# Optimization experiments

Measured on AMD Instinct MI355X. Metric: run time of the kernel, lower is better.

Reference implementation:

```python
import jax, jax.numpy as jnp
import numpy as np

MOE_TOP_K = 2
MOE_GATE_NORM_STD = 1.0  # moe_gate_norm_std


def setup_inputs() -> dict:
    key = jax.random.key(0)
    k1, k2, k3, k4 = jax.random.split(key, 4)
    T, D, E = 16384, 2048, 8
    return {
        "x": jax.random.normal(k1, (T, D), dtype=jnp.float32),
        "wg_weight": jax.random.normal(k2, (E, D), dtype=jnp.float32) * 0.02,
        "gate_map_weight": jax.random.normal(k3, (E, E), dtype=jnp.float32) * 0.1,
        "gate_residual": jax.random.normal(k4, (T, E), dtype=jnp.float32),
    }


def reference(x, wg_weight, gate_map_weight, gate_residual):
    # Router GEMM in fp32 (module force-casts wg and input to float32)
    logits = jnp.einsum("td,ed->te", x.astype(jnp.float32), wg_weight)  # [T, E]
    # gate_residual path: gate_map Linear(E, E, bias=False)
    logits = logits + jnp.einsum("te,fe->tf", gate_residual, gate_map_weight)

    num_experts = wg_weight.shape[0]
    # gating(): moe_use_mixtral_gating=False, moe_use_logits_norm=True
    # torch.std is unbiased (ddof=1)
    logits_std = jnp.std(logits, axis=1, keepdims=True, ddof=1)
    probs = jax.nn.softmax(logits / (logits_std / MOE_GATE_NORM_STD), axis=1)
    gates, indices = jax.lax.top_k(probs, MOE_TOP_K)  # [T, K]
    # zero out routing to the last expert, then renormalize
    gates = jnp.where(indices == num_experts - 1, jnp.zeros_like(gates), gates)
    gates = gates / jnp.sum(gates, axis=1, keepdims=True)
    # Dense equivalent of the per-expert nonzero-gather dict: (indices, gates)
    # fully determines expert_info[e] = (tokens where indices==e, matching gates).
    return gates, indices, logits
```

## Files before the change

### kernel.cpp

```cpp
#include <hip/hip_runtime.h>
#include <hip/hip_bf16.h>
#include <stdint.h>


#define TOKENS_PER_WAVE 4
#define WAVES_PER_BLOCK 4
#define TOKENS_PER_BLOCK (TOKENS_PER_WAVE * WAVES_PER_BLOCK)
#define DCONST 2048
#define HALF_D 1024

__device__ __forceinline__ unsigned long long shfl_xor_u64(unsigned long long v, int m) {
    int lo = __shfl_xor((int)(uint32_t)v, m, 64);
    int hi = __shfl_xor((int)(uint32_t)(v >> 32), m, 64);
    return ((unsigned long long)(uint32_t)hi << 32) | (unsigned long long)(uint32_t)lo;
}

__global__ __launch_bounds__(256, 4)
void router_kernel(const float* __restrict__ x,
                   const float* __restrict__ wg,
                   const float* __restrict__ gm,
                   const float* __restrict__ gr,
                   float* __restrict__ out,
                   int T)
{
    const int wave = threadIdx.x >> 6;
    const int lane = threadIdx.x & 63;
    const int t0   = blockIdx.x * TOKENS_PER_BLOCK + wave * TOKENS_PER_WAVE;

    __shared__ float swg[8 * HALF_D];

    float acc[32];
    #pragma unroll
    for (int v = 0; v < 32; ++v) acc[v] = 0.f;

    const float* xw = x + (size_t)t0 * DCONST + (lane << 2);
    const float* wl = swg + (lane << 2);

    float4 xa[TOKENS_PER_WAVE], xb[TOKENS_PER_WAVE];

    #define LOADX(buf, g)                                                     \
        { _Pragma("unroll")                                                   \
          for (int tt = 0; tt < TOKENS_PER_WAVE; ++tt)                        \
              buf[tt] = *(const float4*)(xw + tt * DCONST + (g) * 256); }

    #define COMPUTE(j, buf)                                                   \
        { _Pragma("unroll")                                                   \
          for (int e = 0; e < 8; ++e) {                                       \
              const float4 wf = *(const float4*)(wl + e * HALF_D + (j) * 256);\
              _Pragma("unroll")                                               \
              for (int tt = 0; tt < TOKENS_PER_WAVE; ++tt) {                  \
                  acc[tt * 8 + e] += buf[tt].x * wf.x;                        \
                  acc[tt * 8 + e] += buf[tt].y * wf.y;                        \
                  acc[tt * 8 + e] += buf[tt].z * wf.z;                        \
                  acc[tt * 8 + e] += buf[tt].w * wf.w;                        \
              }                                                               \
          } }

    #pragma unroll 1
    for (int p = 0; p < 2; ++p) {
        if (p) __syncthreads();
        {
            const float4* src = (const float4*)wg;
            float4*       dst = (float4*)swg;
            #pragma unroll
            for (int i = 0; i < 8; ++i) {
                const int idx = threadIdx.x + i * 256;
                const int e   = idx >> 8;
                const int c4  = idx & 255;
                dst[idx] = src[e * 512 + p * 256 + c4];
            }
        }
        __syncthreads();

        const int g0 = p * 4;
        LOADX(xa, g0);
        LOADX(xb, g0 + 1);
        COMPUTE(0, xa);
        LOADX(xa, g0 + 2);
        COMPUTE(1, xb);
        LOADX(xb, g0 + 3);
        COMPUTE(2, xa);
        COMPUTE(3, xb);
    }

    #pragma unroll
    for (int m = 1; m < 32; m <<= 1) {
        const bool up = (lane & m) != 0;
        #pragma unroll
        for (int v = 0; v < 32; v += 2 * m) {
            const float keep = up ? acc[v + m] : acc[v];
            const float send = up ? acc[v] : acc[v + m];
            const float got  = __shfl_xor(send, m, 64);
            acc[v] = keep + got;
        }
    }
    float logit = acc[0] + __shfl_xor(acc[0], 32, 64);

    const int vv = lane & 31;
    const int tt = vv >> 3;
    const int f  = vv & 7;
    const int t  = t0 + tt;

    const float4 ga = *(const float4*)(gr + (size_t)t * 8);
    const float4 gb = *(const float4*)(gr + (size_t)t * 8 + 4);
    const float4 ma = *(const float4*)(gm + f * 8);
    const float4 mb = *(const float4*)(gm + f * 8 + 4);
    logit += ga.x * ma.x + ga.y * ma.y + ga.z * ma.z + ga.w * ma.w
           + gb.x * mb.x + gb.y * mb.y + gb.z * mb.z + gb.w * mb.w;

    if (lane < 32)
        out[(size_t)4 * T + (size_t)t0 * 8 + lane] = logit;

    float s = logit;
    s += __shfl_xor(s, 1, 64);
    s += __shfl_xor(s, 2, 64);
    s += __shfl_xor(s, 4, 64);
    const float mean = s * 0.125f;
    float d2 = (logit - mean) * (logit - mean);
    d2 += __shfl_xor(d2, 1, 64);
    d2 += __shfl_xor(d2, 2, 64);
    d2 += __shfl_xor(d2, 4, 64);
    const float stdv = sqrtf(d2 / 7.0f);

    uint32_t ob = __float_as_uint(logit);
    ob = (ob & 0x80000000u) ? ~ob : (ob | 0x80000000u);
    unsigned long long k1 = ((unsigned long long)ob << 8) | (unsigned long long)(7 - f);
    unsigned long long k2 = 0ull;
    #pragma unroll
    for (int m = 1; m <= 4; m <<= 1) {
        const unsigned long long o1 = shfl_xor_u64(k1, m);
        const unsigned long long o2 = shfl_xor_u64(k2, m);
        const unsigned long long hi = k1 > o1 ? k1 : o1;
        const unsigned long long lo = k1 > o1 ? o1 : k1;
        const unsigned long long so = k2 > o2 ? k2 : o2;
        k1 = hi;
        k2 = lo > so ? lo : so;
    }
    const int i1 = 7 - (int)(k1 & 0xFFull);
    const int i2 = 7 - (int)(k2 & 0xFFull);
    uint32_t b1 = (uint32_t)(k1 >> 8), b2 = (uint32_t)(k2 >> 8);
    b1 = (b1 & 0x80000000u) ? (b1 ^ 0x80000000u) : ~b1;
    b2 = (b2 & 0x80000000u) ? (b2 ^ 0x80000000u) : ~b2;
    const float l1 = __uint_as_float(b1);
    const float l2 = __uint_as_float(b2);

    float g0, g1;
    if (i1 == 7)      { g0 = 0.f; g1 = 1.f; }
    else if (i2 == 7) { g0 = 1.f; g1 = 0.f; }
    else {
        const float p = 1.0f / (1.0f + __expf(-(l1 - l2) / stdv));
        g0 = p; g1 = 1.0f - p;
    }

    if (lane < 32) {
        if (f == 0) out[(size_t)2 * t]             = g0;
        if (f == 1) out[(size_t)2 * t + 1]         = g1;
        if (f == 2) out[(size_t)2 * T + 2 * t]     = (float)i1;
        if (f == 3) out[(size_t)2 * T + 2 * t + 1] = (float)i2;
    }
}

extern "C" void kernel_launch(void* const* d_in, const int* in_sizes, int n_in,
                              void* d_out, int out_size, void* d_ws, size_t ws_size,
                              hipStream_t stream) {
    const float* x  = (const float*)d_in[0];
    const float* wg = (const float*)d_in[1];
    const float* gm = (const float*)d_in[2];
    const float* gr = (const float*)d_in[3];
    const int T = in_sizes[0] / DCONST;
    const int blocks = T / TOKENS_PER_BLOCK;
    router_kernel<<<blocks, 256, 0, stream>>>(x, wg, gm, gr, (float*)d_out, T);
}
```

Baseline: 225.3 us.

## Load router weights directly from global memory instead of staging in LDS

```diff
diff --git a/kernel.cpp b/kernel.cpp
--- a/kernel.cpp
+++ b/kernel.cpp
@@ -3,11 +3,7 @@
 #include <stdint.h>
 
 
-#define TOKENS_PER_WAVE 4
-#define WAVES_PER_BLOCK 4
-#define TOKENS_PER_BLOCK (TOKENS_PER_WAVE * WAVES_PER_BLOCK)
 #define DCONST 2048
-#define HALF_D 1024
 
 __device__ __forceinline__ unsigned long long shfl_xor_u64(unsigned long long v, int m) {
     int lo = __shfl_xor((int)(uint32_t)v, m, 64);
@@ -15,7 +11,7 @@
     return ((unsigned long long)(uint32_t)hi << 32) | (unsigned long long)(uint32_t)lo;
 }
 
-__global__ __launch_bounds__(256, 4)
+__global__ __launch_bounds__(256, 3)
 void router_kernel(const float* __restrict__ x,
                    const float* __restrict__ wg,
                    const float* __restrict__ gm,
@@ -25,62 +21,50 @@
 {
     const int wave = threadIdx.x >> 6;
     const int lane = threadIdx.x & 63;
-    const int t0   = blockIdx.x * TOKENS_PER_BLOCK + wave * TOKENS_PER_WAVE;
+    const int t0   = (blockIdx.x * 4 + wave) * 4;
 
-    __shared__ float swg[8 * HALF_D];
+    const float* xp = x  + (size_t)t0 * DCONST + (lane << 2);
+    const float* wp = wg + (lane << 2);
 
     float acc[32];
     #pragma unroll
     for (int v = 0; v < 32; ++v) acc[v] = 0.f;
 
-    const float* xw = x + (size_t)t0 * DCONST + (lane << 2);
-    const float* wl = swg + (lane << 2);
+    float4 xa[4], xb[4], w8[8];
 
-    float4 xa[TOKENS_PER_WAVE], xb[TOKENS_PER_WAVE];
+    #define LOADX(buf, j)                                                     \
+        { _Pragma("unroll")                                                   \
+          for (int i = 0; i < 4; ++i)                                         \
+              buf[i] = *(const float4*)(xp + (size_t)i * DCONST + (j) * 256); }
 
-    #define LOADX(buf, g)                                                     \
+    #define LOADW(j)                                                          \
         { _Pragma("unroll")                                                   \
-          for (int tt = 0; tt < TOKENS_PER_WAVE; ++tt)                        \
-              buf[tt] = *(const float4*)(xw + tt * DCONST + (g) * 256); }
+          for (int e = 0; e < 8; ++e)                                         \
+              w8[e] = *(const float4*)(wp + (size_t)e * DCONST + (j) * 256); }
 
-    #define COMPUTE(j, buf)                                                   \
+    #define FMA4(buf)                                                         \
         { _Pragma("unroll")                                                   \
-          for (int e = 0; e < 8; ++e) {                                       \
-              const float4 wf = *(const float4*)(wl + e * HALF_D + (j) * 256);\
+          for (int i = 0; i < 4; ++i) {                                       \
               _Pragma("unroll")                                               \
-              for (int tt = 0; tt < TOKENS_PER_WAVE; ++tt) {                  \
-                  acc[tt * 8 + e] += buf[tt].x * wf.x;                        \
-                  acc[tt * 8 + e] += buf[tt].y * wf.y;                        \
-                  acc[tt * 8 + e] += buf[tt].z * wf.z;                        \
-                  acc[tt * 8 + e] += buf[tt].w * wf.w;                        \
+              for (int e = 0; e < 8; ++e) {                                   \
+                  float a = acc[i * 8 + e];                                   \
+                  a += buf[i].x * w8[e].x;                                    \
+                  a += buf[i].y * w8[e].y;                                    \
+                  a += buf[i].z * w8[e].z;                                    \
+                  a += buf[i].w * w8[e].w;                                    \
+                  acc[i * 8 + e] = a;                                         \
               }                                                               \
           } }
 
+    LOADX(xa, 0);
     #pragma unroll 1
-    for (int p = 0; p < 2; ++p) {
-        if (p) __syncthreads();
-        {
-            const float4* src = (const float4*)wg;
-            float4*       dst = (float4*)swg;
-            #pragma unroll
-            for (int i = 0; i < 8; ++i) {
-                const int idx = threadIdx.x + i * 256;
-                const int e   = idx >> 8;
-                const int c4  = idx & 255;
-                dst[idx] = src[e * 512 + p * 256 + c4];
-            }
-        }
-        __syncthreads();
-
-        const int g0 = p * 4;
-        LOADX(xa, g0);
-        LOADX(xb, g0 + 1);
-        COMPUTE(0, xa);
-        LOADX(xa, g0 + 2);
-        COMPUTE(1, xb);
-        LOADX(xb, g0 + 3);
-        COMPUTE(2, xa);
-        COMPUTE(3, xb);
+    for (int j = 0; j < 8; j += 2) {
+        LOADW(j);
+        LOADX(xb, j + 1);
+        FMA4(xa);
+        LOADW(j + 1);
+        if (j + 2 < 8) LOADX(xa, j + 2);
+        FMA4(xb);
     }
 
     #pragma unroll
@@ -109,7 +93,7 @@
            + gb.x * mb.x + gb.y * mb.y + gb.z * mb.z + gb.w * mb.w;
 
     if (lane < 32)
-        out[(size_t)4 * T + (size_t)t0 * 8 + lane] = logit;
+        out[(size_t)4 * T + (size_t)t0 * 8 + vv] = logit;
 
     float s = logit;
     s += __shfl_xor(s, 1, 64);
@@ -168,6 +152,6 @@
     const float* gm = (const float*)d_in[2];
     const float* gr = (const float*)d_in[3];
     const int T = in_sizes[0] / DCONST;
-    const int blocks = T / TOKENS_PER_BLOCK;
+    const int blocks = T / 16;
     router_kernel<<<blocks, 256, 0, stream>>>(x, wg, gm, gr, (float*)d_out, T);
 }
```

Result: faster. 205.4 us (-8.8%).
